# Performance work log

Hardware: AMD Instinct MI355X
Metric: run time of the kernel (lower is better)

Reference implementation:

```python
import jax, jax.numpy as jnp
import numpy as np

B, L, D, H = 2, 2048, 1024, 16
DH = D // H


def setup_inputs() -> dict:
    key = jax.random.key(0)
    ks = jax.random.split(key, 5)
    bound = 1.0 / D ** 0.5
    x = jax.random.normal(ks[0], (B, L, D), dtype=jnp.float32)
    # causal mask: 0 means masked out
    mask = jnp.tril(jnp.ones((L, L), dtype=jnp.int32))[None].repeat(B, axis=0)
    Wq = jax.random.uniform(ks[1], (D, D), jnp.float32, -bound, bound)
    Wk = jax.random.uniform(ks[2], (D, D), jnp.float32, -bound, bound)
    Wv = jax.random.uniform(ks[3], (D, D), jnp.float32, -bound, bound)
    Wo = jax.random.uniform(ks[4], (D, D), jnp.float32, -bound, bound)
    return {"x": x, "mask": mask, "Wq": Wq, "Wk": Wk, "Wv": Wv, "Wo": Wo}


def _split_heads(t):
    # (B, L, D) -> (B, H, L, DH)
    b, l, _ = t.shape
    return t.reshape(b, l, H, DH).transpose(0, 2, 1, 3)


def reference(x, mask, Wq, Wk, Wv, Wo):
    # projections: torch Linear does x @ W.T with W:(out,in)
    q = _split_heads(x @ Wq.T)  # (B,H,L,DH)
    k = _split_heads(x @ Wk.T)
    v = _split_heads(x @ Wv.T)
    scores = jnp.einsum('bhqd,bhkd->bhqk', q, k) / jnp.sqrt(jnp.float32(DH))
    m = mask[:, None, :, :]  # (B,1,L,L)
    scores = jnp.where(m == 0, jnp.float32(-jnp.inf), scores)
    attn = jax.nn.softmax(scores, axis=-1)
    out = jnp.einsum('bhqk,bhkd->bhqd', attn, v)  # (B,H,L,DH)
    out = out.transpose(0, 2, 1, 3).reshape(x.shape[0], x.shape[1], D)
    return out @ Wo.T
```

## Files before the change

kernel.cpp:

```cpp
#include <hip/hip_runtime.h>
#include <stdint.h>


typedef unsigned short u16;
typedef __attribute__((ext_vector_type(8))) short short8;
typedef __attribute__((ext_vector_type(4))) float f32x4;
typedef __attribute__((ext_vector_type(4))) unsigned int uint4v;

#define NEG_BIG (-1e30f)
#define QSCALE 0.18033688011112042f

__device__ __forceinline__ f32x4 mfma16(short8 a, short8 b, f32x4 c) {
    return __builtin_amdgcn_mfma_f32_16x16x32_bf16(a, b, c, 0, 0, 0);
}

__device__ __forceinline__ u16 f2bf(float f) {
    uint32_t u = __float_as_uint(f);
    u += 0x7fffu + ((u >> 16) & 1u);
    return (u16)(u >> 16);
}

__device__ __forceinline__ float bf2f(u16 v) {
    return __uint_as_float((uint32_t)v << 16);
}

#if __has_builtin(__builtin_amdgcn_cvt_pk_bf16_f32)
__device__ __forceinline__ unsigned int f2bf_pk(float a, float b) {
    return __builtin_bit_cast(unsigned int, __builtin_amdgcn_cvt_pk_bf16_f32(a, b));
}
#else
__device__ __forceinline__ unsigned int f2bf_pk(float a, float b) {
    return (unsigned int)f2bf(a) | ((unsigned int)f2bf(b) << 16);
}
#endif

__device__ __forceinline__ void load_lds_16B(const u16* g, u16* lds_base) {
    __builtin_amdgcn_global_load_lds(
        (__attribute__((address_space(1))) void*)(uintptr_t)(const void*)g,
        (__attribute__((address_space(3))) void*)lds_base,
        16, 0, 0);
}

__global__ __launch_bounds__(256) void cvt_kernel(
    const float* __restrict__ x, const float* __restrict__ wq, const float* __restrict__ wk,
    const float* __restrict__ wv, const float* __restrict__ wo, u16* __restrict__ dst)
{
    const int gid = blockIdx.x * 256 + threadIdx.x;
    const float* src; size_t off;
    if (gid < 524288)      { src = x;  off = (size_t)gid * 8; }
    else if (gid < 655360) { src = wq; off = (size_t)(gid - 524288) * 8; }
    else if (gid < 786432) { src = wk; off = (size_t)(gid - 655360) * 8; }
    else if (gid < 917504) { src = wv; off = (size_t)(gid - 786432) * 8; }
    else                   { src = wo; off = (size_t)(gid - 917504) * 8; }
    float4 a = *(const float4*)(src + off);
    float4 b = *(const float4*)(src + off + 4);
    uint4v u = { f2bf_pk(a.x, a.y), f2bf_pk(a.z, a.w),
                 f2bf_pk(b.x, b.y), f2bf_pk(b.z, b.w) };
    *(uint4v*)(dst + (size_t)gid * 8) = u;
}

template<bool SWAP>
__device__ __forceinline__ void gemm_bt_128x128_bk64(
    const u16* __restrict__ A, const u16* __restrict__ Bw,
    u16* at, u16* bt, int m0, int n0, f32x4 acc[4][4])
{
    const int tid  = threadIdx.x;
    const int w    = tid >> 6, lane = tid & 63;
    const int quad = lane >> 4, l15 = lane & 15;
    const int wm   = (w >> 1) * 64, wn = (w & 1) * 64;
    const int srow = lane >> 3;
    const int sch  = lane & 7;

    for (int k0 = 0; k0 < 1024; k0 += 64) {
#pragma unroll
        for (int c = 0; c < 4; ++c) {
            int row = w * 32 + c * 8 + srow;
            int g   = sch ^ (row & 7);
            load_lds_16B(A  + (size_t)(m0 + row) * 1024 + k0 + g * 8, at + (w * 32 + c * 8) * 64);
            load_lds_16B(Bw + (size_t)(n0 + row) * 1024 + k0 + g * 8, bt + (w * 32 + c * 8) * 64);
        }
        __syncthreads();
#pragma unroll
        for (int ks = 0; ks < 2; ++ks) {
            short8 af[4], bf[4];
#pragma unroll
            for (int rf = 0; rf < 4; ++rf) {
                int ra = wm + rf * 16 + l15, pa = (ks * 4 + quad) ^ (ra & 7);
                af[rf] = *(const short8*)(at + ra * 64 + pa * 8);
                int rb = wn + rf * 16 + l15, pb = (ks * 4 + quad) ^ (rb & 7);
                bf[rf] = *(const short8*)(bt + rb * 64 + pb * 8);
            }
#pragma unroll
            for (int rf = 0; rf < 4; ++rf)
#pragma unroll
                for (int cf = 0; cf < 4; ++cf) {
                    if constexpr (SWAP)
                        acc[rf][cf] = mfma16(bf[rf], af[cf], acc[rf][cf]);
                    else
                        acc[rf][cf] = mfma16(af[rf], bf[cf], acc[rf][cf]);
                }
        }
        __syncthreads();
    }
}

__global__ __launch_bounds__(256, 3) void qkv_gemm(
    const u16* __restrict__ xb, const u16* __restrict__ Wq, const u16* __restrict__ Wk,
    const u16* __restrict__ Wv, u16* __restrict__ qbuf, u16* __restrict__ kbuf,
    u16* __restrict__ vtbuf)
{
    __shared__ __align__(16) u16 at[128 * 64];
    __shared__ __align__(16) u16 bt[128 * 64];
    const int m0  = blockIdx.x * 128;
    const int by  = blockIdx.y;
    const int sel = by >> 3;
    const int n0  = (by & 7) * 128;
    const u16* Wsel = sel == 0 ? Wq : (sel == 1 ? Wk : Wv);

    f32x4 acc[4][4];
    const f32x4 z = {0.f, 0.f, 0.f, 0.f};
#pragma unroll
    for (int i = 0; i < 4; ++i)
#pragma unroll
        for (int j = 0; j < 4; ++j) acc[i][j] = z;

    const int tid  = threadIdx.x, w = tid >> 6, lane = tid & 63;
    const int quad = lane >> 4, l15 = lane & 15;
    const int wm   = (w >> 1) * 64, wn = (w & 1) * 64;

    if (sel < 2) {
        gemm_bt_128x128_bk64<true>(xb, Wsel, at, bt, m0, n0, acc);
        u16* dst = sel == 0 ? qbuf : kbuf;
        const float scl = sel == 0 ? QSCALE : 1.0f;
        const int b = m0 >> 11;
        const int h = (n0 + wn) >> 6;
#pragma unroll
        for (int rf = 0; rf < 4; ++rf)
#pragma unroll
            for (int cf = 0; cf < 4; ++cf) {
                int l = (m0 & 2047) + wm + cf * 16 + l15;
                ushort4 pk;
                pk.x = f2bf(acc[rf][cf][0] * scl);
                pk.y = f2bf(acc[rf][cf][1] * scl);
                pk.z = f2bf(acc[rf][cf][2] * scl);
                pk.w = f2bf(acc[rf][cf][3] * scl);
                *(ushort4*)(dst + (((size_t)(b * 16 + h)) * 2048 + l) * 64
                            + rf * 16 + quad * 4) = pk;
            }
    } else {
        gemm_bt_128x128_bk64<false>(xb, Wsel, at, bt, m0, n0, acc);
#pragma unroll
        for (int rf = 0; rf < 4; ++rf)
#pragma unroll
            for (int cf = 0; cf < 4; ++cf) {
                int n = n0 + wn + cf * 16 + l15;
                int h = n >> 6, dh = n & 63;
                int m = m0 + wm + rf * 16 + quad * 4;
                int b = m >> 11, l = m & 2047;
                int lp = (l & ~31) | (quad << 3) | (((l >> 4) & 1) << 2);
                ushort4 pk;
                pk.x = f2bf(acc[rf][cf][0]);
                pk.y = f2bf(acc[rf][cf][1]);
                pk.z = f2bf(acc[rf][cf][2]);
                pk.w = f2bf(acc[rf][cf][3]);
                *(ushort4*)(vtbuf + (((size_t)(b * 16 + h)) * 64 + dh) * 2048 + lp) = pk;
            }
    }
}

struct Chain {
    short8 qf[2];
    f32x4  o[4];
    float  l;
};

__global__ __launch_bounds__(256, 4) void attn_kernel(
    const u16* __restrict__ qbuf, const u16* __restrict__ kbuf,
    const u16* __restrict__ vtbuf, u16* __restrict__ attn,
    u16* __restrict__ po, float* __restrict__ pl)
{
    __shared__ __align__(16) u16 smem[16384];

    const int tid  = threadIdx.x, w = tid >> 6, lane = tid & 63;
    const int quad = lane >> 4, l15 = lane & 15;
    const int e3   = l15 & 7;
    const int fid  = (int)(blockIdx.y * 32 + blockIdx.x);
    const int u_   = ((fid & 7) << 7) | (fid >> 3);
    const int bh   = u_ >> 5;
    const int a    = (u_ >> 1) & 15;
    const int role = u_ & 1;
    const int jqS  = a, jqB = 31 - a;

    const u16* qbase = qbuf  + (size_t)bh * 2048 * 64;
    const u16* kbase = kbuf  + (size_t)bh * 2048 * 64;
    const u16* vbase = vtbuf + (size_t)bh * 64 * 2048;
    const int b = bh >> 4, h = bh & 15;
    const int rowi = w * 16 + l15;

    u16* const bk0 = smem + l15 * 64 + ((quad ^ e3) * 8);
    u16* const bk1 = smem + l15 * 64 + (((4 + quad) ^ e3) * 8);

    const int srow = w * 16 + (lane >> 3);
    const int gofs = ((lane & 7) ^ (lane >> 3)) * 8;
    const u16* kg0 = kbase + (size_t)srow * 64 + gofs;
    const u16* kg1 = kg0 + 8 * 64;
    const u16* vg0 = vbase + (size_t)srow * 2048 + gofs;
    const u16* vg1 = vg0 + 8 * 2048;
    u16* const kd0 = smem + w * 16 * 64;
    u16* const kd1 = kd0 + 512;
    u16* const vd0 = kd0 + 8192;
    u16* const vd1 = kd1 + 8192;

    short8 ones;
#pragma unroll
    for (int j = 0; j < 8; ++j) ones[j] = (short)0x3F80;

    const f32x4 z = {0.f, 0.f, 0.f, 0.f};

    auto stage = [&](int buf) {
        const int bo = buf << 12;
        load_lds_16B(kg0, kd0 + bo);
        load_lds_16B(kg1, kd1 + bo);
        load_lds_16B(vg0, vd0 + bo);
        load_lds_16B(vg1, vd1 + bo);
        kg0 += 4096; kg1 += 4096; vg0 += 64; vg1 += 64;
    };

    auto load_q = [&](int jq, Chain& c) {
        int qw = jq * 64 + w * 16;
#pragma unroll
        for (int ks = 0; ks < 2; ++ks)
            c.qf[ks] = *(const short8*)(qbase + (size_t)(qw + l15) * 64 + ks * 32 + quad * 8);
        c.l = 0.f;
#pragma unroll
        for (int df = 0; df < 4; ++df) c.o[df] = z;
    };

    auto visit = [&](const u16* c0, const u16* c1, Chain& c, int k0, int qrow, bool diag) {
        f32x4 st[4] = {z, z, z, z};
        __builtin_amdgcn_s_setprio(1);
#pragma unroll
        for (int nf = 0; nf < 4; ++nf)
            st[nf] = mfma16(*(const short8*)(c0 + nf * 1024), c.qf[0], st[nf]);
#pragma unroll
        for (int nf = 0; nf < 4; ++nf)
            st[nf] = mfma16(*(const short8*)(c1 + nf * 1024), c.qf[1], st[nf]);
        __builtin_amdgcn_s_setprio(0);
        if (diag) {
            const int thr = qrow - k0 - quad * 4;
#pragma unroll
            for (int nf = 0; nf < 4; ++nf)
#pragma unroll
                for (int r = 0; r < 4; ++r)
                    if (nf * 16 + r > thr) st[nf][r] = NEG_BIG;
        }
        uint4v pu0 = { f2bf_pk(exp2f(st[0][0]), exp2f(st[0][1])),
                       f2bf_pk(exp2f(st[0][2]), exp2f(st[0][3])),
                       f2bf_pk(exp2f(st[1][0]), exp2f(st[1][1])),
                       f2bf_pk(exp2f(st[1][2]), exp2f(st[1][3])) };
        uint4v pu1 = { f2bf_pk(exp2f(st[2][0]), exp2f(st[2][1])),
                       f2bf_pk(exp2f(st[2][2]), exp2f(st[2][3])),
                       f2bf_pk(exp2f(st[3][0]), exp2f(st[3][1])),
                       f2bf_pk(exp2f(st[3][2]), exp2f(st[3][3])) };
        short8 pv0 = __builtin_bit_cast(short8, pu0);
        short8 pv1 = __builtin_bit_cast(short8, pu1);
        f32x4 ls = z;
        __builtin_amdgcn_s_setprio(1);
        ls = mfma16(ones, pv0, ls);
#pragma unroll
        for (int df = 0; df < 4; ++df)
            c.o[df] = mfma16(*(const short8*)(c0 + 8192 + df * 1024), pv0, c.o[df]);
        ls = mfma16(ones, pv1, ls);
#pragma unroll
        for (int df = 0; df < 4; ++df)
            c.o[df] = mfma16(*(const short8*)(c1 + 8192 + df * 1024), pv1, c.o[df]);
        __builtin_amdgcn_s_setprio(0);
        c.l += ls[0];
    };

    if (role == 0) {
        Chain cS, cB;
        load_q(jqS, cS);
        load_q(jqB, cB);
        const int tS = a, tB = 15 - a;
        const int T0 = tS > tB ? tS : tB;
        stage(0);
        for (int t = 0; t <= T0; ++t) {
            __syncthreads();
            if (t < T0) stage((t + 1) & 1);
            const int bo = (t & 1) << 12;
            const u16* c0 = bk0 + bo;
            const u16* c1 = bk1 + bo;
            if (t <= tB) visit(c0, c1, cB, 0, 0, false);
            if (t <= tS) visit(c0, c1, cS, t * 64, jqS * 64 + rowi, t == tS);
        }
        {
            float inv = 1.f / cS.l;
            int qrow = jqS * 64 + rowi;
            u16* obase = attn + ((size_t)(b * 2048 + qrow)) * 1024 + h * 64 + quad * 4;
#pragma unroll
            for (int df = 0; df < 4; ++df) {
                uint2 pk2 = { f2bf_pk(cS.o[df][0] * inv, cS.o[df][1] * inv),
                              f2bf_pk(cS.o[df][2] * inv, cS.o[df][3] * inv) };
                *(uint2*)(obase + df * 16) = pk2;
            }
        }
        {
            int p = (bh * 16 + a) * 2 + 0;
            u16* ob = po + (size_t)p * 4096 + rowi * 64 + quad * 4;
#pragma unroll
            for (int df = 0; df < 4; ++df) {
                uint2 pk2 = { f2bf_pk(cB.o[df][0], cB.o[df][1]),
                              f2bf_pk(cB.o[df][2], cB.o[df][3]) };
                *(uint2*)(ob + df * 16) = pk2;
            }
            if (quad == 0) pl[p * 64 + rowi] = cB.l;
        }
    } else {
        Chain cB;
        load_q(jqB, cB);
        const int tb = 16 - a, te = 31 - a;
        kg0 += (size_t)tb * 4096; kg1 += (size_t)tb * 4096;
        vg0 += tb * 64; vg1 += tb * 64;
        stage(tb & 1);
        for (int t = tb; t <= te; ++t) {
            __syncthreads();
            if (t < te) stage((t + 1) & 1);
            const int bo = (t & 1) << 12;
            visit(bk0 + bo, bk1 + bo, cB, t * 64, jqB * 64 + rowi, t == te);
        }
        int p = (bh * 16 + a) * 2 + 1;
        u16* ob = po + (size_t)p * 4096 + rowi * 64 + quad * 4;
#pragma unroll
        for (int df = 0; df < 4; ++df) {
            uint2 pk2 = { f2bf_pk(cB.o[df][0], cB.o[df][1]),
                          f2bf_pk(cB.o[df][2], cB.o[df][3]) };
            *(uint2*)(ob + df * 16) = pk2;
        }
        if (quad == 0) pl[p * 64 + rowi] = cB.l;
    }
}

__global__ __launch_bounds__(256) void merge_kernel(
    const u16* __restrict__ po, const float* __restrict__ pl,
    u16* __restrict__ attn)
{
    const int u   = blockIdx.x;
    const int bh  = u >> 4, a = u & 15;
    const int b   = bh >> 4, h = bh & 15;
    const int jqB = 31 - a;
    const int row = threadIdx.x >> 2, seg = threadIdx.x & 3;
    const int p0  = u * 2, p1 = u * 2 + 1;

    float inv = 1.f / (pl[p0 * 64 + row] + pl[p1 * 64 + row]);

    const u16* o0p = po + (size_t)p0 * 4096 + row * 64 + seg * 16;
    const u16* o1p = po + (size_t)p1 * 4096 + row * 64 + seg * 16;
    short8 o0a = *(const short8*)(o0p);
    short8 o0b = *(const short8*)(o0p + 8);
    short8 o1a = *(const short8*)(o1p);
    short8 o1b = *(const short8*)(o1p + 8);

    float r[16];
#pragma unroll
    for (int j = 0; j < 8; ++j) {
        r[j]     = (bf2f((u16)o0a[j]) + bf2f((u16)o1a[j])) * inv;
        r[8 + j] = (bf2f((u16)o0b[j]) + bf2f((u16)o1b[j])) * inv;
    }
    uint4v pka = { f2bf_pk(r[0], r[1]), f2bf_pk(r[2], r[3]), f2bf_pk(r[4], r[5]), f2bf_pk(r[6], r[7]) };
    uint4v pkb = { f2bf_pk(r[8], r[9]), f2bf_pk(r[10], r[11]), f2bf_pk(r[12], r[13]), f2bf_pk(r[14], r[15]) };
    u16* dst = attn + ((size_t)(b * 2048 + jqB * 64 + row)) * 1024 + h * 64 + seg * 16;
    *(uint4v*)(dst)     = pka;
    *(uint4v*)(dst + 8) = pkb;
}

__global__ __launch_bounds__(256, 4) void oproj_gemm(
    const u16* __restrict__ attn, const u16* __restrict__ Wo, float* __restrict__ out)
{
    __shared__ __align__(16) u16 at[64 * 64];
    __shared__ __align__(16) u16 bt[64 * 64];
    const int m0 = blockIdx.x * 64;
    const int n0 = blockIdx.y * 64;

    const int tid  = threadIdx.x, w = tid >> 6, lane = tid & 63;
    const int quad = lane >> 4, l15 = lane & 15;
    const int wm   = (w >> 1) * 32, wn = (w & 1) * 32;
    const int srow = lane >> 3, sch = lane & 7;

    f32x4 acc[2][2];
    const f32x4 z = {0.f, 0.f, 0.f, 0.f};
#pragma unroll
    for (int i = 0; i < 2; ++i)
#pragma unroll
        for (int j = 0; j < 2; ++j) acc[i][j] = z;

    for (int k0 = 0; k0 < 1024; k0 += 64) {
#pragma unroll
        for (int c = 0; c < 2; ++c) {
            int row = w * 16 + c * 8 + srow;
            int g   = sch ^ (row & 7);
            load_lds_16B(attn + (size_t)(m0 + row) * 1024 + k0 + g * 8, at + (w * 16 + c * 8) * 64);
            load_lds_16B(Wo   + (size_t)(n0 + row) * 1024 + k0 + g * 8, bt + (w * 16 + c * 8) * 64);
        }
        __syncthreads();
#pragma unroll
        for (int ks = 0; ks < 2; ++ks) {
            short8 af[2], bf[2];
#pragma unroll
            for (int rf = 0; rf < 2; ++rf) {
                int ra = wm + rf * 16 + l15, pa = (ks * 4 + quad) ^ (ra & 7);
                af[rf] = *(const short8*)(at + ra * 64 + pa * 8);
                int rb = wn + rf * 16 + l15, pb = (ks * 4 + quad) ^ (rb & 7);
                bf[rf] = *(const short8*)(bt + rb * 64 + pb * 8);
            }
#pragma unroll
            for (int rf = 0; rf < 2; ++rf)
#pragma unroll
                for (int cf = 0; cf < 2; ++cf)
                    acc[rf][cf] = mfma16(af[rf], bf[cf], acc[rf][cf]);
        }
        __syncthreads();
    }

#pragma unroll
    for (int rf = 0; rf < 2; ++rf)
#pragma unroll
        for (int cf = 0; cf < 2; ++cf) {
            int n = n0 + wn + cf * 16 + l15;
#pragma unroll
            for (int r = 0; r < 4; ++r) {
                int m = m0 + wm + rf * 16 + quad * 4 + r;
                out[(size_t)m * 1024 + n] = acc[rf][cf][r];
            }
        }
}

extern "C" void kernel_launch(void* const* d_in, const int* in_sizes, int n_in,
                              void* d_out, int out_size, void* d_ws, size_t ws_size,
                              hipStream_t stream) {
    const float* x  = (const float*)d_in[0];
    const float* Wq = (const float*)d_in[2];
    const float* Wk = (const float*)d_in[3];
    const float* Wv = (const float*)d_in[4];
    const float* Wo = (const float*)d_in[5];

    u16* ws    = (u16*)d_ws;
    const size_t M = 1024 * 1024;
    u16* qbuf  = ws;
    u16* kbuf  = ws + 4 * M;
    u16* vtb   = ws + 8 * M;
    u16* attnb = ws + 12 * M;
    u16* cvtb  = ws + 16 * M;
    u16* xb    = cvtb;
    u16* wqb   = cvtb + 4 * M;
    u16* wkb   = cvtb + 5 * M;
    u16* wvb   = cvtb + 6 * M;
    u16* wob   = cvtb + 7 * M;
    float* out = (float*)d_out;

    u16*   po = cvtb;
    float* plv = (float*)(cvtb + 4 * M);

    cvt_kernel<<<4096, 256, 0, stream>>>(x, Wq, Wk, Wv, Wo, cvtb);
    qkv_gemm<<<dim3(32, 24), 256, 0, stream>>>(xb, wqb, wkb, wvb, qbuf, kbuf, vtb);
    attn_kernel<<<dim3(32, 32), 256, 0, stream>>>(qbuf, kbuf, vtb, attnb, po, plv);
    merge_kernel<<<512, 256, 0, stream>>>(po, plv, attnb);
    oproj_gemm<<<dim3(64, 16), 256, 0, stream>>>(attnb, wob, out);
}
```

Measured before the change: 189.8 us.

## Fuse split-KV merge into output projection GEMM A-tile loading

Removes the separate merge kernel and performs the combination of the two partial attention outputs inside the output-projection GEMM while staging the A tile into LDS. Rows from the split query blocks read both partials, scale by the precomputed inverse row sums, and write bf16 directly into the swizzled LDS tile. This saves a launch and the round trip of the merged attention buffer through global memory. The merge work is repeated for every N-block, and the loads are synchronous instead of direct-to-LDS, which adds load latency and redundant reads.

```diff
diff --git a/kernel.cpp b/kernel.cpp
--- a/kernel.cpp
+++ b/kernel.cpp
@@ -341,44 +341,14 @@
     }
 }
 
-__global__ __launch_bounds__(256) void merge_kernel(
-    const u16* __restrict__ po, const float* __restrict__ pl,
-    u16* __restrict__ attn)
-{
-    const int u   = blockIdx.x;
-    const int bh  = u >> 4, a = u & 15;
-    const int b   = bh >> 4, h = bh & 15;
-    const int jqB = 31 - a;
-    const int row = threadIdx.x >> 2, seg = threadIdx.x & 3;
-    const int p0  = u * 2, p1 = u * 2 + 1;
-
-    float inv = 1.f / (pl[p0 * 64 + row] + pl[p1 * 64 + row]);
-
-    const u16* o0p = po + (size_t)p0 * 4096 + row * 64 + seg * 16;
-    const u16* o1p = po + (size_t)p1 * 4096 + row * 64 + seg * 16;
-    short8 o0a = *(const short8*)(o0p);
-    short8 o0b = *(const short8*)(o0p + 8);
-    short8 o1a = *(const short8*)(o1p);
-    short8 o1b = *(const short8*)(o1p + 8);
-
-    float r[16];
-#pragma unroll
-    for (int j = 0; j < 8; ++j) {
-        r[j]     = (bf2f((u16)o0a[j]) + bf2f((u16)o1a[j])) * inv;
-        r[8 + j] = (bf2f((u16)o0b[j]) + bf2f((u16)o1b[j])) * inv;
-    }
-    uint4v pka = { f2bf_pk(r[0], r[1]), f2bf_pk(r[2], r[3]), f2bf_pk(r[4], r[5]), f2bf_pk(r[6], r[7]) };
-    uint4v pkb = { f2bf_pk(r[8], r[9]), f2bf_pk(r[10], r[11]), f2bf_pk(r[12], r[13]), f2bf_pk(r[14], r[15]) };
-    u16* dst = attn + ((size_t)(b * 2048 + jqB * 64 + row)) * 1024 + h * 64 + seg * 16;
-    *(uint4v*)(dst)     = pka;
-    *(uint4v*)(dst + 8) = pkb;
-}
-
 __global__ __launch_bounds__(256, 4) void oproj_gemm(
-    const u16* __restrict__ attn, const u16* __restrict__ Wo, float* __restrict__ out)
+    const u16* __restrict__ attnb, const u16* __restrict__ po, const float* __restrict__ pl,
+    const u16* __restrict__ Wo, float* __restrict__ out)
 {
     __shared__ __align__(16) u16 at[64 * 64];
     __shared__ __align__(16) u16 bt[64 * 64];
+    __shared__ float invl[1024];
+
     const int m0 = blockIdx.x * 64;
     const int n0 = blockIdx.y * 64;
 
@@ -387,6 +357,28 @@
     const int wm   = (w >> 1) * 32, wn = (w & 1) * 32;
     const int srow = lane >> 3, sch = lane & 7;
 
+    const int b   = m0 >> 11;
+    const int jq  = (m0 & 2047) >> 6;
+    const bool big = jq >= 16;
+    const int a   = 31 - jq;
+
+    if (big) {
+        int h  = tid >> 4;
+        int r4 = (tid & 15) * 4;
+        int p0 = ((b * 16 + h) * 16 + a) * 2;
+#pragma unroll
+        for (int j = 0; j < 4; ++j) {
+            int row = r4 + j;
+            invl[h * 64 + row] = 1.f / (pl[p0 * 64 + row] + pl[(p0 + 1) * 64 + row]);
+        }
+        __syncthreads();
+    }
+
+    const int brow = tid >> 2;
+    const int bcs  = (tid & 3) * 16;
+    const int bg0  = (bcs >> 3) ^ (brow & 7);
+    const int bg1  = ((bcs >> 3) + 1) ^ (brow & 7);
+
     f32x4 acc[2][2];
     const f32x4 z = {0.f, 0.f, 0.f, 0.f};
 #pragma unroll
@@ -394,13 +386,43 @@
 #pragma unroll
         for (int j = 0; j < 2; ++j) acc[i][j] = z;
 
-    for (int k0 = 0; k0 < 1024; k0 += 64) {
+    for (int t = 0; t < 16; ++t) {
+        const int k0 = t * 64;
+        if (!big) {
+#pragma unroll
+            for (int c = 0; c < 2; ++c) {
+                int row = w * 16 + c * 8 + srow;
+                int g   = sch ^ (row & 7);
+                load_lds_16B(attnb + (size_t)(m0 + row) * 1024 + k0 + g * 8,
+                             at + (w * 16 + c * 8) * 64);
+            }
+        } else {
+            size_t pb = ((size_t)(((b * 16 + t) * 16 + a) * 2)) * 4096
+                      + (size_t)brow * 64 + bcs;
+            short8 o0a = *(const short8*)(po + pb);
+            short8 o0b = *(const short8*)(po + pb + 8);
+            short8 o1a = *(const short8*)(po + pb + 4096);
+            short8 o1b = *(const short8*)(po + pb + 4096 + 8);
+            float iv = invl[t * 64 + brow];
+            float r0[8], r1[8];
+#pragma unroll
+            for (int j = 0; j < 8; ++j) {
+                r0[j] = (bf2f((u16)o0a[j]) + bf2f((u16)o1a[j])) * iv;
+                r1[j] = (bf2f((u16)o0b[j]) + bf2f((u16)o1b[j])) * iv;
+            }
+            uint4v pka = { f2bf_pk(r0[0], r0[1]), f2bf_pk(r0[2], r0[3]),
+                           f2bf_pk(r0[4], r0[5]), f2bf_pk(r0[6], r0[7]) };
+            uint4v pkb = { f2bf_pk(r1[0], r1[1]), f2bf_pk(r1[2], r1[3]),
+                           f2bf_pk(r1[4], r1[5]), f2bf_pk(r1[6], r1[7]) };
+            *(uint4v*)(at + brow * 64 + bg0 * 8) = pka;
+            *(uint4v*)(at + brow * 64 + bg1 * 8) = pkb;
+        }
 #pragma unroll
         for (int c = 0; c < 2; ++c) {
             int row = w * 16 + c * 8 + srow;
             int g   = sch ^ (row & 7);
-            load_lds_16B(attn + (size_t)(m0 + row) * 1024 + k0 + g * 8, at + (w * 16 + c * 8) * 64);
-            load_lds_16B(Wo   + (size_t)(n0 + row) * 1024 + k0 + g * 8, bt + (w * 16 + c * 8) * 64);
+            load_lds_16B(Wo + (size_t)(n0 + row) * 1024 + k0 + g * 8,
+                         bt + (w * 16 + c * 8) * 64);
         }
         __syncthreads();
 #pragma unroll
@@ -410,8 +432,8 @@
             for (int rf = 0; rf < 2; ++rf) {
                 int ra = wm + rf * 16 + l15, pa = (ks * 4 + quad) ^ (ra & 7);
                 af[rf] = *(const short8*)(at + ra * 64 + pa * 8);
-                int rb = wn + rf * 16 + l15, pb = (ks * 4 + quad) ^ (rb & 7);
-                bf[rf] = *(const short8*)(bt + rb * 64 + pb * 8);
+                int rb = wn + rf * 16 + l15, pb2 = (ks * 4 + quad) ^ (rb & 7);
+                bf[rf] = *(const short8*)(bt + rb * 64 + pb2 * 8);
             }
 #pragma unroll
             for (int rf = 0; rf < 2; ++rf)
@@ -464,6 +486,5 @@
     cvt_kernel<<<4096, 256, 0, stream>>>(x, Wq, Wk, Wv, Wo, cvtb);
     qkv_gemm<<<dim3(32, 24), 256, 0, stream>>>(xb, wqb, wkb, wvb, qbuf, kbuf, vtb);
     attn_kernel<<<dim3(32, 32), 256, 0, stream>>>(qbuf, kbuf, vtb, attnb, po, plv);
-    merge_kernel<<<512, 256, 0, stream>>>(po, plv, attnb);
-    oproj_gemm<<<dim3(64, 16), 256, 0, stream>>>(attnb, wob, out);
-}
+    oproj_gemm<<<dim3(64, 16), 256, 0, stream>>>(attnb, po, plv, wob, out);
+}
```

After: 196.9 us. 3.8% more time.
